# Performance work log

Hardware: AMD Instinct MI355X
Metric: run time of the kernel (lower is better)

Reference implementation:

```python
import jax, jax.numpy as jnp
import numpy as np

H = 2048  # hidden_size
I = 8192  # intermediate_size
B, S = 4, 2048


def setup_inputs() -> dict:
    key = jax.random.key(0)
    ks = jax.random.split(key, 8)
    scale = 1.0 / np.sqrt(H)
    scale_i = 1.0 / np.sqrt(I)
    x = jax.random.normal(ks[0], (B, S, H), dtype=jnp.float32)
    mask = jax.random.randint(ks[1], (B, S), 0, 2) > 0  # bool per-token routing
    # torch nn.Linear weights are [out_features, in_features]
    w1 = jax.random.normal(ks[2], (I, H), dtype=jnp.float32) * scale
    w2 = jax.random.normal(ks[3], (H, I), dtype=jnp.float32) * scale_i
    w3 = jax.random.normal(ks[4], (I, H), dtype=jnp.float32) * scale
    u1 = jax.random.normal(ks[5], (I, H), dtype=jnp.float32) * scale
    u2 = jax.random.normal(ks[6], (H, I), dtype=jnp.float32) * scale_i
    u3 = jax.random.normal(ks[7], (I, H), dtype=jnp.float32) * scale
    return {"x": x, "mask": mask, "w1": w1, "w2": w2, "w3": w3,
            "u1": u1, "u2": u2, "u3": u3}


def reference(x, mask, w1, w2, w3, u1, u2, u3):
    # branch 1 SwiGLU: silu(x @ w1^T) * (x @ w3^T), then w2
    proj1 = jax.nn.silu(jnp.einsum('bsh,ih->bsi', x, w1)) * jnp.einsum('bsh,ih->bsi', x, w3)
    proj2 = jax.nn.silu(jnp.einsum('bsh,ih->bsi', x, u1)) * jnp.einsum('bsh,ih->bsi', x, u3)
    out1 = jnp.einsum('bsi,hi->bsh', proj1, w2)
    out2 = jnp.einsum('bsi,hi->bsh', proj2, u2)
    m = mask[:, :, None]
    return jnp.where(m, out1, out2)
```

## Files before the change

kernel.cpp:

```cpp
#include <hip/hip_runtime.h>
#include <hip/hip_bf16.h>
#include <stdint.h>

#define DIM_H 2048
#define DIM_I 8192
#define TOKENS 8192
#define RB256 34
#define CROWS (RB256*256)

typedef __attribute__((ext_vector_type(8))) short bf16x8;
typedef __attribute__((ext_vector_type(4))) float f32x4;

#define MF(a,b,c) __builtin_amdgcn_mfma_f32_16x16x32_bf16((a),(b),(c),0,0,0)

__device__ __forceinline__ unsigned short f2bf(float f) {
    union { float f; unsigned u; } v; v.f = f;
    return (unsigned short)((v.u + 0x7FFF + ((v.u >> 16) & 1)) >> 16);
}

__global__ __launch_bounds__(256) void cvt_kernel(const float* __restrict__ in,
                                                  unsigned short* __restrict__ out,
                                                  int n4) {
    int stride = gridDim.x * blockDim.x;
    for (int j = blockIdx.x * blockDim.x + threadIdx.x; j < n4; j += stride) {
        float4 v = reinterpret_cast<const float4*>(in)[j];
        ushort4 o;
        o.x = f2bf(v.x); o.y = f2bf(v.y); o.z = f2bf(v.z); o.w = f2bf(v.w);
        reinterpret_cast<ushort4*>(out)[j] = o;
    }
}

__global__ __launch_bounds__(256) void cvt2_kernel(const float* __restrict__ in0,
                                                   unsigned short* __restrict__ out0,
                                                   const float* __restrict__ in1,
                                                   unsigned short* __restrict__ out1,
                                                   int n4) {
    const int half = gridDim.x >> 1;
    const bool lo = ((int)blockIdx.x < half);
    const float* in = lo ? in0 : in1;
    unsigned short* out = lo ? out0 : out1;
    const int bid = lo ? (int)blockIdx.x : (int)blockIdx.x - half;
    int stride = half * blockDim.x;
    for (int j = bid * blockDim.x + threadIdx.x; j < n4; j += stride) {
        float4 v = reinterpret_cast<const float4*>(in)[j];
        ushort4 o;
        o.x = f2bf(v.x); o.y = f2bf(v.y); o.z = f2bf(v.z); o.w = f2bf(v.w);
        reinterpret_cast<ushort4*>(out)[j] = o;
    }
}

__global__ __launch_bounds__(256) void cvt13x2_kernel(const float* __restrict__ w1,
                                                      const float* __restrict__ w3,
                                                      unsigned short* __restrict__ W13,
                                                      const float* __restrict__ u1,
                                                      const float* __restrict__ u3,
                                                      unsigned short* __restrict__ U13,
                                                      int n4) {
    const int half = gridDim.x >> 1;
    const bool lo = ((int)blockIdx.x < half);
    const float* a1 = lo ? w1 : u1;
    const float* a3 = lo ? w3 : u3;
    unsigned short* ob = lo ? W13 : U13;
    const int bid = lo ? (int)blockIdx.x : (int)blockIdx.x - half;
    int stride = half * blockDim.x;
    for (int j = bid * blockDim.x + threadIdx.x; j < n4; j += stride) {
        int flat = j << 2;
        int R = flat >> 11;
        int col = flat & 2047;
        int orow = ((R >> 4) << 5) | (R & 15);
        float4 v1 = reinterpret_cast<const float4*>(a1)[j];
        float4 v3 = reinterpret_cast<const float4*>(a3)[j];
        ushort4 o1, o3;
        o1.x=f2bf(v1.x); o1.y=f2bf(v1.y); o1.z=f2bf(v1.z); o1.w=f2bf(v1.w);
        o3.x=f2bf(v3.x); o3.y=f2bf(v3.y); o3.z=f2bf(v3.z); o3.w=f2bf(v3.w);
        *reinterpret_cast<ushort4*>(&ob[(size_t)orow * DIM_H + col]) = o1;
        *reinterpret_cast<ushort4*>(&ob[(size_t)(orow + 16) * DIM_H + col]) = o3;
    }
}

__global__ __launch_bounds__(256) void compact_kernel(const int* __restrict__ mask,
                                                      int* __restrict__ idx,
                                                      int* __restrict__ hdr) {
    __shared__ int cnt[256];
    const int t = threadIdx.x;
    const int base = t * 32;
    unsigned bits = 0;
#pragma unroll
    for (int j = 0; j < 32; ++j)
        if (mask[base + j] != 0) bits |= (1u << j);
    const int c = __popc(bits);
    cnt[t] = c;
    __syncthreads();
    for (int off = 1; off < 256; off <<= 1) {
        int v = cnt[t];
        int add = (t >= off) ? cnt[t - off] : 0;
        __syncthreads();
        cnt[t] = v + add;
        __syncthreads();
    }
    const int Mw  = cnt[255];
    const int MwP = (Mw + 255) & ~255;
    const int Mu  = TOKENS - Mw;
    const int MuP = (Mu + 255) & ~255;

    for (int j = t; j < CROWS; j += 256) idx[j] = -1;
    __syncthreads();

    int pw = cnt[t] - c;
    int pz = base - pw;
#pragma unroll
    for (int j = 0; j < 32; ++j) {
        int tok = base + j;
        if ((bits >> j) & 1) idx[pw++] = tok;
        else                 idx[MwP + pz++] = tok;
    }
    if (t == 0) {
        hdr[0] = MwP >> 8;
        hdr[1] = (MwP + MuP) >> 8;
        hdr[2] = Mw;
        hdr[3] = Mu;
    }
}


#define LDF4(D0,D1,D2,D3, SB, RB) do { \
    const unsigned short* _sl = &smem[(SB)]; \
    D0 = *reinterpret_cast<const bf16x8*>(&_sl[((RB) +  0)*32 + c16r]); \
    D1 = *reinterpret_cast<const bf16x8*>(&_sl[((RB) + 16)*32 + c16r]); \
    D2 = *reinterpret_cast<const bf16x8*>(&_sl[((RB) + 32)*32 + c16r]); \
    D3 = *reinterpret_cast<const bf16x8*>(&_sl[((RB) + 48)*32 + c16r]); \
} while(0)

#define LDF2(D0,D1, SB, RB) do { \
    const unsigned short* _sl = &smem[(SB)]; \
    D0 = *reinterpret_cast<const bf16x8*>(&_sl[((RB) +  0)*32 + c16r]); \
    D1 = *reinterpret_cast<const bf16x8*>(&_sl[((RB) + 16)*32 + c16r]); \
} while(0)

#define STAGE2(UB_, S0_, S1_, KOFS_) do { \
    __builtin_amdgcn_global_load_lds((const __attribute__((address_space(1))) void*)((S0_) + (KOFS_)), \
        (__attribute__((address_space(3))) void*)&smem[(UB_) + wave*512], 16, 0, 0); \
    __builtin_amdgcn_global_load_lds((const __attribute__((address_space(1))) void*)((S1_) + (KOFS_)), \
        (__attribute__((address_space(3))) void*)&smem[(UB_) + 4096 + wave*512], 16, 0, 0); \
} while(0)

#define STAGE1(UB_, S0_, KOFS_) \
    __builtin_amdgcn_global_load_lds((const __attribute__((address_space(1))) void*)((S0_) + (KOFS_)), \
        (__attribute__((address_space(3))) void*)&smem[(UB_) + wave*512], 16, 0, 0)

#define MFMA32_G1() do { \
  acc[0][0]=MF(af0,bfr0,acc[0][0]); acc[0][1]=MF(af0,bfr1,acc[0][1]); acc[0][2]=MF(af0,bfr2,acc[0][2]); acc[0][3]=MF(af0,bfr3,acc[0][3]); \
  acc[1][0]=MF(af1,bfr0,acc[1][0]); acc[1][1]=MF(af1,bfr1,acc[1][1]); acc[1][2]=MF(af1,bfr2,acc[1][2]); acc[1][3]=MF(af1,bfr3,acc[1][3]); \
  acc[2][0]=MF(af2,bfr0,acc[2][0]); acc[2][1]=MF(af2,bfr1,acc[2][1]); acc[2][2]=MF(af2,bfr2,acc[2][2]); acc[2][3]=MF(af2,bfr3,acc[2][3]); \
  acc[3][0]=MF(af3,bfr0,acc[3][0]); acc[3][1]=MF(af3,bfr1,acc[3][1]); acc[3][2]=MF(af3,bfr2,acc[3][2]); acc[3][3]=MF(af3,bfr3,acc[3][3]); \
  acc[4][0]=MF(af4,bfr0,acc[4][0]); acc[4][1]=MF(af4,bfr1,acc[4][1]); acc[4][2]=MF(af4,bfr2,acc[4][2]); acc[4][3]=MF(af4,bfr3,acc[4][3]); \
  acc[5][0]=MF(af5,bfr0,acc[5][0]); acc[5][1]=MF(af5,bfr1,acc[5][1]); acc[5][2]=MF(af5,bfr2,acc[5][2]); acc[5][3]=MF(af5,bfr3,acc[5][3]); \
  acc[6][0]=MF(af6,bfr0,acc[6][0]); acc[6][1]=MF(af6,bfr1,acc[6][1]); acc[6][2]=MF(af6,bfr2,acc[6][2]); acc[6][3]=MF(af6,bfr3,acc[6][3]); \
  acc[7][0]=MF(af7,bfr0,acc[7][0]); acc[7][1]=MF(af7,bfr1,acc[7][1]); acc[7][2]=MF(af7,bfr2,acc[7][2]); acc[7][3]=MF(af7,bfr3,acc[7][3]); \
} while(0)

__global__ __launch_bounds__(512, 2) void gemm1_kernel(
    const unsigned short* __restrict__ xb,
    const unsigned short* __restrict__ W13,
    const unsigned short* __restrict__ U13,
    const int* __restrict__ idx, const int* __restrict__ hdr,
    unsigned short* __restrict__ P)
{
    __shared__ __align__(16) unsigned short smem[65536];
    const int wB  = hdr[0];
    const int rbT = hdr[1];
    const int nwg = gridDim.x;
    const int q8  = nwg >> 3;
    const int swzb = ((int)blockIdx.x & 7) * q8 + ((int)blockIdx.x >> 3);
    const int rb = swzb % RB256;
    const int bx = swzb / RB256;
    if (rb >= rbT) return;
    const unsigned short* Bm = (rb < wB) ? W13 : U13;
    const int bm0 = rb << 8;
    const int bn0 = bx << 8;

    const int tid  = threadIdx.x;
    const int lane = tid & 63;
    const int wave = tid >> 6;
    const int wrM = wave >> 2;
    const int wcN = wave & 3;
    const int rAb = wrM * 128 + (lane & 15);
    const int rBb = wcN * 64 + (lane & 15);
    const int c16r = (((lane >> 4) ^ ((lane >> 1) & 3))) << 3;

    const int p0 = tid, p1 = 512 + tid;
    const int r0 = p0 >> 2, r1 = p1 >> 2;
    const int c0 = ((p0 & 3) ^ ((r0 >> 1) & 3)) << 3;
    const int c1 = ((p1 & 3) ^ ((r1 >> 1) & 3)) << 3;
    int t0 = idx[bm0 + r0]; if (t0 < 0) t0 = 0;
    int t1 = idx[bm0 + r1]; if (t1 < 0) t1 = 0;
    const unsigned short* sa0 = xb + (size_t)t0 * DIM_H + c0;
    const unsigned short* sa1 = xb + (size_t)t1 * DIM_H + c1;
    const unsigned short* sb0 = Bm + (size_t)(bn0 + r0) * DIM_H + c0;
    const unsigned short* sb1 = Bm + (size_t)(bn0 + r1) * DIM_H + c1;

    f32x4 acc[8][4] = {};
    bf16x8 af0, af1, af2, af3, af4, af5, af6, af7, bfr0, bfr1, bfr2, bfr3;

    STAGE2(0,     sa0, sa1, 0);
    STAGE2(16384, sb0, sb1, 0);
    STAGE2(8192,  sa0, sa1, 32);
    STAGE2(24576, sb0, sb1, 32);
    STAGE2(32768, sa0, sa1, 64);
    STAGE2(49152, sb0, sb1, 64);
    asm volatile("s_waitcnt vmcnt(8)" ::: "memory");
    __builtin_amdgcn_s_barrier();
    int ko = 96;
    for (int t = 0; t < 32; ++t) {
        const int cur = (t & 1) << 15;
        const int nxt = cur ^ 32768;
        LDF4(af0,af1,af2,af3, cur,          rAb);
        LDF4(af4,af5,af6,af7, cur,          rAb + 64);
        LDF4(bfr0,bfr1,bfr2,bfr3, cur + 16384, rBb);
        STAGE2(nxt + 8192,  sa0, sa1, ko);
        STAGE2(nxt + 24576, sb0, sb1, ko);
        __builtin_amdgcn_s_setprio(1);
        MFMA32_G1();
        __builtin_amdgcn_s_setprio(0);
        asm volatile("s_waitcnt vmcnt(8)" ::: "memory");
        __builtin_amdgcn_s_barrier();
        LDF4(af0,af1,af2,af3, cur + 8192,   rAb);
        LDF4(af4,af5,af6,af7, cur + 8192,   rAb + 64);
        LDF4(bfr0,bfr1,bfr2,bfr3, cur + 24576, rBb);
        STAGE2(cur,         sa0, sa1, ko + 32);
        STAGE2(cur + 16384, sb0, sb1, ko + 32);
        ko += 64;
        __builtin_amdgcn_s_setprio(1);
        MFMA32_G1();
        __builtin_amdgcn_s_setprio(0);
        asm volatile("s_waitcnt vmcnt(8)" ::: "memory");
        __builtin_amdgcn_s_barrier();
    }

    const int crow = (lane >> 4) << 2;
    const int ccol = lane & 15;
    unsigned short* Pw = P + (size_t)(bm0 + wrM * 128) * DIM_I
                           + (size_t)bx * 128 + wcN * 32 + ccol;
#pragma unroll
    for (int m = 0; m < 8; ++m) {
#pragma unroll
        for (int q = 0; q < 2; ++q) {
            f32x4 h1 = acc[m][2 * q];
            f32x4 h3 = acc[m][2 * q + 1];
#pragma unroll
            for (int r = 0; r < 4; ++r) {
                float a = h1[r];
                float p = a * (1.0f / (1.0f + __expf(-a))) * h3[r];
                Pw[(size_t)(m * 16 + crow + r) * DIM_I + q * 16] = f2bf(p);
            }
        }
    }
}

#define MFMA16Q(AF0,AF1,AF2,AF3, B0,B1,B2,B3) do { \
  acc[0][0]=MF(AF0,B0,acc[0][0]); acc[0][1]=MF(AF0,B1,acc[0][1]); acc[0][2]=MF(AF0,B2,acc[0][2]); acc[0][3]=MF(AF0,B3,acc[0][3]); \
  acc[1][0]=MF(AF1,B0,acc[1][0]); acc[1][1]=MF(AF1,B1,acc[1][1]); acc[1][2]=MF(AF1,B2,acc[1][2]); acc[1][3]=MF(AF1,B3,acc[1][3]); \
  acc[2][0]=MF(AF2,B0,acc[2][0]); acc[2][1]=MF(AF2,B1,acc[2][1]); acc[2][2]=MF(AF2,B2,acc[2][2]); acc[2][3]=MF(AF2,B3,acc[2][3]); \
  acc[3][0]=MF(AF3,B0,acc[3][0]); acc[3][1]=MF(AF3,B1,acc[3][1]); acc[3][2]=MF(AF3,B2,acc[3][2]); acc[3][3]=MF(AF3,B3,acc[3][3]); \
} while(0)

__global__ __launch_bounds__(512, 2) void gemm2_kernel(
    const unsigned short* __restrict__ P,
    const unsigned short* __restrict__ w2b, const unsigned short* __restrict__ u2b,
    const int* __restrict__ idx, const int* __restrict__ hdr,
    float* __restrict__ out)
{
    __shared__ __align__(16) unsigned short smem[73728];
    const int wB2  = hdr[0] * 2;
    const int rbT2 = hdr[1] * 2;
    const int nwg = gridDim.x;
    const int q8  = nwg >> 3;
    const int swz = ((int)blockIdx.x & 7) * q8 + ((int)blockIdx.x >> 3);
    const int rb = swz & 63;
    const int bx = swz >> 6;
    if (rb >= rbT2) return;
    const unsigned short* Bm = (rb < wB2) ? w2b : u2b;
    const int bm0 = rb << 7;
    const int bn0 = bx << 8;

    const int tid  = threadIdx.x;
    const int lane = tid & 63;
    const int wave = tid >> 6;
    const int wrM = wave >> 2;
    const int wcN = wave & 3;
    const int rAb = wrM * 64 + (lane & 15);
    const int rBb = wcN * 64 + (lane & 15);
    const int c16r = (((lane >> 4) ^ ((lane >> 1) & 3))) << 3;

    const int r0 = tid >> 2, r1 = 128 + r0;
    const int c0 = ((tid & 3) ^ ((r0 >> 1) & 3)) << 3;
    const int c1 = ((tid & 3) ^ ((r1 >> 1) & 3)) << 3;
    const unsigned short* sa0 = P  + (size_t)(bm0 + r0) * DIM_I + c0;
    const unsigned short* sb0 = Bm + (size_t)(bn0 + r0) * DIM_I + c0;
    const unsigned short* sb1 = Bm + (size_t)(bn0 + r1) * DIM_I + c1;

    f32x4 acc[4][4] = {};
    bf16x8 af0, af1, af2, af3, af4, af5, af6, af7;
    bf16x8 bfr0, bfr1, bfr2, bfr3, bfr4, bfr5, bfr6, bfr7;

    STAGE1(0,     sa0, 0);
    STAGE1(4096,  sa0, 32);
    STAGE2(8192,  sb0, sb1, 0);
    STAGE2(16384, sb0, sb1, 32);
    STAGE1(24576,         sa0, 64);
    STAGE1(24576 + 4096,  sa0, 96);
    STAGE2(24576 + 8192,  sb0, sb1, 64);
    STAGE2(24576 + 16384, sb0, sb1, 96);
    asm volatile("s_waitcnt vmcnt(6)" ::: "memory");
    __builtin_amdgcn_s_barrier();
    int ko = 128, cb = 0;
    for (int t = 0; t < 128; ++t) {
        const int base = cb * 24576;
        int nb = base + 49152; if (nb >= 73728) nb -= 73728;
        LDF4(af0,af1,af2,af3,     base,          rAb);
        LDF4(af4,af5,af6,af7,     base + 4096,   rAb);
        LDF4(bfr0,bfr1,bfr2,bfr3, base + 8192,   rBb);
        LDF4(bfr4,bfr5,bfr6,bfr7, base + 16384,  rBb);
        STAGE1(nb,         sa0, ko);
        STAGE1(nb + 4096,  sa0, ko + 32);
        STAGE2(nb + 8192,  sb0, sb1, ko);
        STAGE2(nb + 16384, sb0, sb1, ko + 32);
        ko += 64;
        __builtin_amdgcn_s_setprio(1);
        MFMA16Q(af0,af1,af2,af3, bfr0,bfr1,bfr2,bfr3);
        MFMA16Q(af4,af5,af6,af7, bfr4,bfr5,bfr6,bfr7);
        __builtin_amdgcn_s_setprio(0);
        asm volatile("s_waitcnt vmcnt(6)" ::: "memory");
        __builtin_amdgcn_s_barrier();
        cb = (cb == 2) ? 0 : cb + 1;
    }

    const int crow = (lane >> 4) << 2;
    const int ccol = lane & 15;
#pragma unroll
    for (int m = 0; m < 4; ++m) {
#pragma unroll
        for (int r = 0; r < 4; ++r) {
            int rowc = bm0 + wrM * 64 + m * 16 + crow + r;
            int g = idx[rowc];
            if (g >= 0) {
                float* op = out + (size_t)g * DIM_H + bn0 + wcN * 64 + ccol;
#pragma unroll
                for (int n = 0; n < 4; ++n) op[n * 16] = acc[m][n][r];
            }
        }
    }
}

__global__ __launch_bounds__(256, 2) void gemm2_tail_kernel(
    const unsigned short* __restrict__ P,
    const unsigned short* __restrict__ w2b, const unsigned short* __restrict__ u2b,
    const int* __restrict__ idx, const int* __restrict__ hdr,
    float* __restrict__ out)
{
    __shared__ __align__(16) unsigned short smem[24576];
    const int wB2  = hdr[0] * 2;
    const int rbT2 = hdr[1] * 2;
    const int b   = (int)blockIdx.x;
    const int bx  = b & 31;
    const int sub = (b >> 5) & 1;
    const int rb  = 64 + (b >> 6);
    if (rb >= rbT2) return;
    const unsigned short* Bm = (rb < wB2) ? w2b : u2b;
    const int bm0 = (rb << 7) + (sub << 6);
    const int bn0 = bx << 6;

    const int tid  = threadIdx.x;
    const int lane = tid & 63;
    const int wave = tid >> 6;
    const int wrM = wave >> 1;
    const int wcN = wave & 1;
    const int rAb = wrM * 32 + (lane & 15);
    const int rBb = wcN * 32 + (lane & 15);
    const int c16r = (((lane >> 4) ^ ((lane >> 1) & 3))) << 3;

    const int r0 = tid >> 2;
    const int c0 = ((tid & 3) ^ ((r0 >> 1) & 3)) << 3;
    const unsigned short* sa0 = P  + (size_t)(bm0 + r0) * DIM_I + c0;
    const unsigned short* sb0 = Bm + (size_t)(bn0 + r0) * DIM_I + c0;

    f32x4 acc[2][2] = {};
    bf16x8 a00, a01, a10, a11, b00, b01, b10, b11;

    STAGE1(0,    sa0, 0);  STAGE1(2048,        sa0, 32);
    STAGE1(4096, sb0, 0);  STAGE1(6144,        sb0, 32);
    STAGE1(8192,  sa0, 64); STAGE1(8192 + 2048, sa0, 96);
    STAGE1(8192 + 4096, sb0, 64); STAGE1(8192 + 6144, sb0, 96);
    asm volatile("s_waitcnt vmcnt(4)" ::: "memory");
    __builtin_amdgcn_s_barrier();
    int ko = 128, cb = 0;
    for (int t = 0; t < 128; ++t) {
        const int base = cb * 8192;
        int nb = base + 16384; if (nb >= 24576) nb -= 24576;
        LDF2(a00,a01, base,        rAb);
        LDF2(a10,a11, base + 2048, rAb);
        LDF2(b00,b01, base + 4096, rBb);
        LDF2(b10,b11, base + 6144, rBb);
        STAGE1(nb,        sa0, ko); STAGE1(nb + 2048, sa0, ko + 32);
        STAGE1(nb + 4096, sb0, ko); STAGE1(nb + 6144, sb0, ko + 32);
        ko += 64;
        __builtin_amdgcn_s_setprio(1);
        acc[0][0]=MF(a00,b00,acc[0][0]); acc[0][1]=MF(a00,b01,acc[0][1]);
        acc[1][0]=MF(a01,b00,acc[1][0]); acc[1][1]=MF(a01,b01,acc[1][1]);
        acc[0][0]=MF(a10,b10,acc[0][0]); acc[0][1]=MF(a10,b11,acc[0][1]);
        acc[1][0]=MF(a11,b10,acc[1][0]); acc[1][1]=MF(a11,b11,acc[1][1]);
        __builtin_amdgcn_s_setprio(0);
        asm volatile("s_waitcnt vmcnt(4)" ::: "memory");
        __builtin_amdgcn_s_barrier();
        cb = (cb == 2) ? 0 : cb + 1;
    }

    const int crow = (lane >> 4) << 2;
    const int ccol = lane & 15;
#pragma unroll
    for (int m = 0; m < 2; ++m) {
#pragma unroll
        for (int r = 0; r < 4; ++r) {
            int rowc = bm0 + wrM * 32 + m * 16 + crow + r;
            int g = idx[rowc];
            if (g >= 0) {
                float* op = out + (size_t)g * DIM_H + bn0 + wcN * 32 + ccol;
#pragma unroll
                for (int n = 0; n < 2; ++n) op[n * 16] = acc[m][n][r];
            }
        }
    }
}

extern "C" void kernel_launch(void* const* d_in, const int* in_sizes, int n_in,
                              void* d_out, int out_size, void* d_ws, size_t ws_size,
                              hipStream_t stream) {
    const float* x    = (const float*)d_in[0];
    const int*   mask = (const int*)d_in[1];
    const float* w1 = (const float*)d_in[2];
    const float* w2 = (const float*)d_in[3];
    const float* w3 = (const float*)d_in[4];
    const float* u1 = (const float*)d_in[5];
    const float* u2 = (const float*)d_in[6];
    const float* u3 = (const float*)d_in[7];
    float* out = (float*)d_out;

    const size_t XN   = (size_t)TOKENS * DIM_H;
    const size_t WN   = (size_t)DIM_I * DIM_H;
    const size_t PN   = (size_t)CROWS * DIM_I;
    const size_t W13N = 2 * WN;

    unsigned short* ws  = (unsigned short*)d_ws;
    unsigned short* xb  = ws;
    unsigned short* Pb  = xb + XN;
    unsigned short* W13 = Pb + PN;
    unsigned short* U13 = W13 + W13N;
    int* idx = (int*)(U13 + W13N);
    int* hdr = idx + CROWS;
    unsigned short* w2b = W13;
    unsigned short* u2b = U13;

    const int cvtBlocks = 2048;
    const int n4 = (int)(WN / 4);

    cvt_kernel   <<<cvtBlocks, 256, 0, stream>>>(x, xb, (int)(XN / 4));
    cvt13x2_kernel<<<2 * cvtBlocks, 256, 0, stream>>>(w1, w3, W13, u1, u3, U13, n4);
    compact_kernel<<<1, 256, 0, stream>>>(mask, idx, hdr);

    gemm1_kernel<<<64 * RB256, 512, 0, stream>>>(xb, W13, U13, idx, hdr, Pb);

    cvt2_kernel<<<2 * cvtBlocks, 256, 0, stream>>>(w2, w2b, u2, u2b, n4);

    gemm2_kernel<<<512, 512, 0, stream>>>(Pb, w2b, u2b, idx, hdr, out);
    gemm2_tail_kernel<<<256, 256, 0, stream>>>(Pb, w2b, u2b, idx, hdr, out);
}
```

Before: 981.3 us.

## Shrink gemm1 M tile to 128 rows with triple-buffered 64-wide K stages

Changes the gate/up GEMM tile from 256x256 to 128x256 rows per workgroup, doubling the grid to 64*68 blocks. The K pipeline moves from double-buffered 32-wide halves to a three-slot ring of 64-wide K stages, with one barrier per iteration. The aim is finer routing granularity, so less padding is wasted on the compacted token rows, and deeper prefetch. The cost is lower arithmetic intensity per tile, since the B tile is reused over half as many rows, plus more LDS use.

```diff
diff --git a/kernel.cpp b/kernel.cpp
--- a/kernel.cpp
+++ b/kernel.cpp
@@ -148,15 +148,11 @@
     __builtin_amdgcn_global_load_lds((const __attribute__((address_space(1))) void*)((S0_) + (KOFS_)), \
         (__attribute__((address_space(3))) void*)&smem[(UB_) + wave*512], 16, 0, 0)
 
-#define MFMA32_G1() do { \
-  acc[0][0]=MF(af0,bfr0,acc[0][0]); acc[0][1]=MF(af0,bfr1,acc[0][1]); acc[0][2]=MF(af0,bfr2,acc[0][2]); acc[0][3]=MF(af0,bfr3,acc[0][3]); \
-  acc[1][0]=MF(af1,bfr0,acc[1][0]); acc[1][1]=MF(af1,bfr1,acc[1][1]); acc[1][2]=MF(af1,bfr2,acc[1][2]); acc[1][3]=MF(af1,bfr3,acc[1][3]); \
-  acc[2][0]=MF(af2,bfr0,acc[2][0]); acc[2][1]=MF(af2,bfr1,acc[2][1]); acc[2][2]=MF(af2,bfr2,acc[2][2]); acc[2][3]=MF(af2,bfr3,acc[2][3]); \
-  acc[3][0]=MF(af3,bfr0,acc[3][0]); acc[3][1]=MF(af3,bfr1,acc[3][1]); acc[3][2]=MF(af3,bfr2,acc[3][2]); acc[3][3]=MF(af3,bfr3,acc[3][3]); \
-  acc[4][0]=MF(af4,bfr0,acc[4][0]); acc[4][1]=MF(af4,bfr1,acc[4][1]); acc[4][2]=MF(af4,bfr2,acc[4][2]); acc[4][3]=MF(af4,bfr3,acc[4][3]); \
-  acc[5][0]=MF(af5,bfr0,acc[5][0]); acc[5][1]=MF(af5,bfr1,acc[5][1]); acc[5][2]=MF(af5,bfr2,acc[5][2]); acc[5][3]=MF(af5,bfr3,acc[5][3]); \
-  acc[6][0]=MF(af6,bfr0,acc[6][0]); acc[6][1]=MF(af6,bfr1,acc[6][1]); acc[6][2]=MF(af6,bfr2,acc[6][2]); acc[6][3]=MF(af6,bfr3,acc[6][3]); \
-  acc[7][0]=MF(af7,bfr0,acc[7][0]); acc[7][1]=MF(af7,bfr1,acc[7][1]); acc[7][2]=MF(af7,bfr2,acc[7][2]); acc[7][3]=MF(af7,bfr3,acc[7][3]); \
+#define MFMA16Q(AF0,AF1,AF2,AF3, B0,B1,B2,B3) do { \
+  acc[0][0]=MF(AF0,B0,acc[0][0]); acc[0][1]=MF(AF0,B1,acc[0][1]); acc[0][2]=MF(AF0,B2,acc[0][2]); acc[0][3]=MF(AF0,B3,acc[0][3]); \
+  acc[1][0]=MF(AF1,B0,acc[1][0]); acc[1][1]=MF(AF1,B1,acc[1][1]); acc[1][2]=MF(AF1,B2,acc[1][2]); acc[1][3]=MF(AF1,B3,acc[1][3]); \
+  acc[2][0]=MF(AF2,B0,acc[2][0]); acc[2][1]=MF(AF2,B1,acc[2][1]); acc[2][2]=MF(AF2,B2,acc[2][2]); acc[2][3]=MF(AF2,B3,acc[2][3]); \
+  acc[3][0]=MF(AF3,B0,acc[3][0]); acc[3][1]=MF(AF3,B1,acc[3][1]); acc[3][2]=MF(AF3,B2,acc[3][2]); acc[3][3]=MF(AF3,B3,acc[3][3]); \
 } while(0)
 
 __global__ __launch_bounds__(512, 2) void gemm1_kernel(
@@ -166,17 +162,17 @@
     const int* __restrict__ idx, const int* __restrict__ hdr,
     unsigned short* __restrict__ P)
 {
-    __shared__ __align__(16) unsigned short smem[65536];
-    const int wB  = hdr[0];
-    const int rbT = hdr[1];
+    __shared__ __align__(16) unsigned short smem[73728];
+    const int wB2  = hdr[0] * 2;
+    const int rbT2 = hdr[1] * 2;
     const int nwg = gridDim.x;
     const int q8  = nwg >> 3;
-    const int swzb = ((int)blockIdx.x & 7) * q8 + ((int)blockIdx.x >> 3);
-    const int rb = swzb % RB256;
-    const int bx = swzb / RB256;
-    if (rb >= rbT) return;
-    const unsigned short* Bm = (rb < wB) ? W13 : U13;
-    const int bm0 = rb << 8;
+    const int swz = ((int)blockIdx.x & 7) * q8 + ((int)blockIdx.x >> 3);
+    const int rb = swz % 68;
+    const int bx = swz / 68;
+    if (rb >= rbT2) return;
+    const unsigned short* Bm = (rb < wB2) ? W13 : U13;
+    const int bm0 = rb << 7;
     const int bn0 = bx << 8;
 
     const int tid  = threadIdx.x;
@@ -184,65 +180,60 @@
     const int wave = tid >> 6;
     const int wrM = wave >> 2;
     const int wcN = wave & 3;
-    const int rAb = wrM * 128 + (lane & 15);
+    const int rAb = wrM * 64 + (lane & 15);
     const int rBb = wcN * 64 + (lane & 15);
     const int c16r = (((lane >> 4) ^ ((lane >> 1) & 3))) << 3;
 
-    const int p0 = tid, p1 = 512 + tid;
-    const int r0 = p0 >> 2, r1 = p1 >> 2;
-    const int c0 = ((p0 & 3) ^ ((r0 >> 1) & 3)) << 3;
-    const int c1 = ((p1 & 3) ^ ((r1 >> 1) & 3)) << 3;
+    const int r0 = tid >> 2, r1 = 128 + r0;
+    const int c0 = ((tid & 3) ^ ((r0 >> 1) & 3)) << 3;
+    const int c1 = ((tid & 3) ^ ((r1 >> 1) & 3)) << 3;
     int t0 = idx[bm0 + r0]; if (t0 < 0) t0 = 0;
-    int t1 = idx[bm0 + r1]; if (t1 < 0) t1 = 0;
     const unsigned short* sa0 = xb + (size_t)t0 * DIM_H + c0;
-    const unsigned short* sa1 = xb + (size_t)t1 * DIM_H + c1;
     const unsigned short* sb0 = Bm + (size_t)(bn0 + r0) * DIM_H + c0;
     const unsigned short* sb1 = Bm + (size_t)(bn0 + r1) * DIM_H + c1;
 
-    f32x4 acc[8][4] = {};
-    bf16x8 af0, af1, af2, af3, af4, af5, af6, af7, bfr0, bfr1, bfr2, bfr3;
-
-    STAGE2(0,     sa0, sa1, 0);
-    STAGE2(16384, sb0, sb1, 0);
-    STAGE2(8192,  sa0, sa1, 32);
-    STAGE2(24576, sb0, sb1, 32);
-    STAGE2(32768, sa0, sa1, 64);
-    STAGE2(49152, sb0, sb1, 64);
-    asm volatile("s_waitcnt vmcnt(8)" ::: "memory");
+    f32x4 acc[4][4] = {};
+    bf16x8 af0, af1, af2, af3, af4, af5, af6, af7;
+    bf16x8 bfr0, bfr1, bfr2, bfr3, bfr4, bfr5, bfr6, bfr7;
+
+    STAGE1(0,     sa0, 0);
+    STAGE1(4096,  sa0, 32);
+    STAGE2(8192,  sb0, sb1, 0);
+    STAGE2(16384, sb0, sb1, 32);
+    STAGE1(24576,         sa0, 64);
+    STAGE1(24576 + 4096,  sa0, 96);
+    STAGE2(24576 + 8192,  sb0, sb1, 64);
+    STAGE2(24576 + 16384, sb0, sb1, 96);
+    asm volatile("s_waitcnt vmcnt(6)" ::: "memory");
     __builtin_amdgcn_s_barrier();
-    int ko = 96;
+    int ko = 128, cb = 0;
     for (int t = 0; t < 32; ++t) {
-        const int cur = (t & 1) << 15;
-        const int nxt = cur ^ 32768;
-        LDF4(af0,af1,af2,af3, cur,          rAb);
-        LDF4(af4,af5,af6,af7, cur,          rAb + 64);
-        LDF4(bfr0,bfr1,bfr2,bfr3, cur + 16384, rBb);
-        STAGE2(nxt + 8192,  sa0, sa1, ko);
-        STAGE2(nxt + 24576, sb0, sb1, ko);
-        __builtin_amdgcn_s_setprio(1);
-        MFMA32_G1();
-        __builtin_amdgcn_s_setprio(0);
-        asm volatile("s_waitcnt vmcnt(8)" ::: "memory");
-        __builtin_amdgcn_s_barrier();
-        LDF4(af0,af1,af2,af3, cur + 8192,   rAb);
-        LDF4(af4,af5,af6,af7, cur + 8192,   rAb + 64);
-        LDF4(bfr0,bfr1,bfr2,bfr3, cur + 24576, rBb);
-        STAGE2(cur,         sa0, sa1, ko + 32);
-        STAGE2(cur + 16384, sb0, sb1, ko + 32);
+        const int base = cb * 24576;
+        int nb = base + 49152; if (nb >= 73728) nb -= 73728;
+        LDF4(af0,af1,af2,af3,     base,          rAb);
+        LDF4(af4,af5,af6,af7,     base + 4096,   rAb);
+        LDF4(bfr0,bfr1,bfr2,bfr3, base + 8192,   rBb);
+        LDF4(bfr4,bfr5,bfr6,bfr7, base + 16384,  rBb);
+        STAGE1(nb,         sa0, ko);
+        STAGE1(nb + 4096,  sa0, ko + 32);
+        STAGE2(nb + 8192,  sb0, sb1, ko);
+        STAGE2(nb + 16384, sb0, sb1, ko + 32);
         ko += 64;
         __builtin_amdgcn_s_setprio(1);
-        MFMA32_G1();
+        MFMA16Q(af0,af1,af2,af3, bfr0,bfr1,bfr2,bfr3);
+        MFMA16Q(af4,af5,af6,af7, bfr4,bfr5,bfr6,bfr7);
         __builtin_amdgcn_s_setprio(0);
-        asm volatile("s_waitcnt vmcnt(8)" ::: "memory");
+        asm volatile("s_waitcnt vmcnt(6)" ::: "memory");
         __builtin_amdgcn_s_barrier();
+        cb = (cb == 2) ? 0 : cb + 1;
     }
 
     const int crow = (lane >> 4) << 2;
     const int ccol = lane & 15;
-    unsigned short* Pw = P + (size_t)(bm0 + wrM * 128) * DIM_I
+    unsigned short* Pw = P + (size_t)(bm0 + wrM * 64) * DIM_I
                            + (size_t)bx * 128 + wcN * 32 + ccol;
 #pragma unroll
-    for (int m = 0; m < 8; ++m) {
+    for (int m = 0; m < 4; ++m) {
 #pragma unroll
         for (int q = 0; q < 2; ++q) {
             f32x4 h1 = acc[m][2 * q];
@@ -256,13 +247,6 @@
         }
     }
 }
-
-#define MFMA16Q(AF0,AF1,AF2,AF3, B0,B1,B2,B3) do { \
-  acc[0][0]=MF(AF0,B0,acc[0][0]); acc[0][1]=MF(AF0,B1,acc[0][1]); acc[0][2]=MF(AF0,B2,acc[0][2]); acc[0][3]=MF(AF0,B3,acc[0][3]); \
-  acc[1][0]=MF(AF1,B0,acc[1][0]); acc[1][1]=MF(AF1,B1,acc[1][1]); acc[1][2]=MF(AF1,B2,acc[1][2]); acc[1][3]=MF(AF1,B3,acc[1][3]); \
-  acc[2][0]=MF(AF2,B0,acc[2][0]); acc[2][1]=MF(AF2,B1,acc[2][1]); acc[2][2]=MF(AF2,B2,acc[2][2]); acc[2][3]=MF(AF2,B3,acc[2][3]); \
-  acc[3][0]=MF(AF3,B0,acc[3][0]); acc[3][1]=MF(AF3,B1,acc[3][1]); acc[3][2]=MF(AF3,B2,acc[3][2]); acc[3][3]=MF(AF3,B3,acc[3][3]); \
-} while(0)
 
 __global__ __launch_bounds__(512, 2) void gemm2_kernel(
     const unsigned short* __restrict__ P,
@@ -467,7 +451,7 @@
     cvt13x2_kernel<<<2 * cvtBlocks, 256, 0, stream>>>(w1, w3, W13, u1, u3, U13, n4);
     compact_kernel<<<1, 256, 0, stream>>>(mask, idx, hdr);
 
-    gemm1_kernel<<<64 * RB256, 512, 0, stream>>>(xb, W13, U13, idx, hdr, Pb);
+    gemm1_kernel<<<64 * 68, 512, 0, stream>>>(xb, W13, U13, idx, hdr, Pb);
 
     cvt2_kernel<<<2 * cvtBlocks, 256, 0, stream>>>(w2, w2b, u2, u2b, n4);
 
```

New measurement: 1.086 ms. +10.7%, slower.
